# Kernel optimization log

Hardware: AMD Instinct MI355X
Metric: run time of the kernel (lower is better)

Reference implementation:

```python
import jax, jax.numpy as jnp
import numpy as np

B, A, N_IN, N_POINTS = 64, 256, 512, 2048


def _sq_cdist(u, v):
    # |u_i - v_j|^2 via expansion, abs() as in the torch original
    d = -2.0 * (u @ v.T) + (u * u).sum(1)[:, None] + (v * v).sum(1)[None, :]
    return jnp.abs(d)


def setup_inputs() -> dict:
    key = jax.random.key(0)
    k1, k2, k3, k4 = jax.random.split(key, 4)
    x = jax.random.normal(k1, (B, A, N_IN), dtype=jnp.float32)
    atom_mask = jax.random.bernoulli(k2, 0.8, (B, A))  # ragged valid-atom mask
    inducing_points = jax.random.normal(k3, (N_POINTS, N_IN), dtype=jnp.float32)
    gamma = (1.0 + 0.25 * jax.random.normal(k4, (N_IN,), dtype=jnp.float32)) * np.sqrt(N_IN).astype(np.float32)
    return {"x": x, "atom_mask": atom_mask, "inducing_points": inducing_points, "gamma": gamma}


def reference(x, atom_mask, inducing_points, gamma):
    b, a, n_in = x.shape
    m = atom_mask.astype(x.dtype)                      # [B, A]
    mf = m[..., None]                                  # [B, A, 1]
    n = m.sum()
    # masked mean / unbiased std over valid atoms (torch .std is ddof=1)
    mean = (x * mf).sum((0, 1)) / n                    # [n_in]
    var = (((x - mean) ** 2) * mf).sum((0, 1)) / (n - 1.0)
    std = jnp.sqrt(var) + 1e-5                         # [n_in]
    xn = (x - mean) / std * mf                         # zero out padded atoms

    g2 = gamma ** 2 + 0.001                            # [n_in]
    z = (xn / g2).reshape(b * a, n_in)                 # [N, n_in]
    zi = inducing_points / g2                          # [M, n_in]

    Kx = jnp.exp(-_sq_cdist(z, zi))                    # [N, M]
    Kind = jnp.exp(-_sq_cdist(zi, zi))                 # [M, M]
    Kinv = jnp.linalg.inv(Kind + 0.05 * jnp.eye(Kind.shape[0], dtype=x.dtype))

    t = Kx @ Kinv                                      # [N, M]
    x_new = ((t @ inducing_points) * std + mean).reshape(b, a, n_in) * mf
    var_out = (1.0 - (t * Kx).sum(-1)).reshape(b, a) * m
    return x_new, var_out
```

## Files before the change

kernel.cpp:

```cpp
#include <hip/hip_runtime.h>
#include <math.h>
#include <stdint.h>

namespace {

constexpr int NROW = 16384;
constexpr int NF   = 512;
constexpr int MIND = 2048;
constexpr float CC = 0.98f;

typedef _Float16 half8 __attribute__((ext_vector_type(8)));
typedef float floatx4 __attribute__((ext_vector_type(4)));

__device__ __forceinline__ void gload16(const void* g, void* l) {
  __builtin_amdgcn_global_load_lds(
      (__attribute__((address_space(1))) void*)g,
      (__attribute__((address_space(3))) void*)l, 16, 0, 0);
}

__global__ __launch_bounds__(256) void stats_kernel(
    const float* __restrict__ x, const int* __restrict__ mask,
    float* __restrict__ sum, float* __restrict__ sumsq, float* __restrict__ cnt)
{
  const int t = threadIdx.x;
  const int row0 = blockIdx.x * 64;
  float s0 = 0.f, s1 = 0.f, q0 = 0.f, q1 = 0.f, c = 0.f;
  for (int r = 0; r < 64; ++r) {
    const int row = row0 + r;
    const float m = (mask[row] != 0) ? 1.f : 0.f;
    const float v0 = x[(size_t)row * NF + t];
    const float v1 = x[(size_t)row * NF + t + 256];
    s0 += m * v0; q0 += m * v0 * v0;
    s1 += m * v1; q1 += m * v1 * v1;
    c += m;
  }
  atomicAdd(&sum[t], s0);        atomicAdd(&sum[t + 256], s1);
  atomicAdd(&sumsq[t], q0);      atomicAdd(&sumsq[t + 256], q1);
  if (t == 0) atomicAdd(cnt, c);
}

__global__ __launch_bounds__(256) void finalize_stats(
    const float* __restrict__ sum, const float* __restrict__ sumsq,
    const float* __restrict__ cnt, const float* __restrict__ gamma,
    float* __restrict__ meanv, float* __restrict__ stdv,
    float* __restrict__ zsv, float* __restrict__ giv)
{
  const int f = blockIdx.x * 256 + threadIdx.x;
  const float n = cnt[0];
  const float mu = sum[f] / n;
  const float var = (sumsq[f] - sum[f] * mu) / (n - 1.0f);
  const float sd = sqrtf(var) + 1e-5f;
  const float g = gamma[f];
  const float g2 = g * g + 0.001f;
  meanv[f] = mu;
  stdv[f]  = sd;
  zsv[f]   = 1.0f / (sd * g2);
  giv[f]   = 1.0f / g2;
}

__global__ __launch_bounds__(256) void make_z(
    const float* __restrict__ x, const int* __restrict__ mask,
    const float* __restrict__ ip, const float* __restrict__ meanv,
    const float* __restrict__ zsv, const float* __restrict__ giv,
    _Float16* __restrict__ Zh, _Float16* __restrict__ Zih,
    float* __restrict__ rnorm, float* __restrict__ cnorm)
{
  const int row = blockIdx.x;
  const int t = threadIdx.x;
  float v0, v1;
  if (row < NROW) {
    const float m = (mask[row] != 0) ? 1.f : 0.f;
    v0 = (x[(size_t)row * NF + t      ] - meanv[t      ]) * zsv[t      ] * m;
    v1 = (x[(size_t)row * NF + t + 256] - meanv[t + 256]) * zsv[t + 256] * m;
    const _Float16 h0 = (_Float16)v0, h1 = (_Float16)v1;
    Zh[(size_t)row * NF + t] = h0;
    Zh[(size_t)row * NF + t + 256] = h1;
    v0 = (float)h0; v1 = (float)h1;
  } else {
    const int r = row - NROW;
    v0 = ip[(size_t)r * NF + t      ] * giv[t      ];
    v1 = ip[(size_t)r * NF + t + 256] * giv[t + 256];
    const _Float16 h0 = (_Float16)v0, h1 = (_Float16)v1;
    Zih[(size_t)r * NF + t] = h0;
    Zih[(size_t)r * NF + t + 256] = h1;
    v0 = (float)h0; v1 = (float)h1;
  }
  float nrm = v0 * v0 + v1 * v1;
  #pragma unroll
  for (int off = 32; off; off >>= 1) nrm += __shfl_xor(nrm, off);
  __shared__ float red[4];
  if ((t & 63) == 0) red[t >> 6] = nrm;
  __syncthreads();
  if (t == 0) {
    const float s = red[0] + red[1] + red[2] + red[3];
    if (row < NROW) rnorm[row] = s; else cnorm[row - NROW] = s;
  }
}

template <int EPI>
__global__ __launch_bounds__(256) void mfma_gemm(
    const _Float16* __restrict__ A, const _Float16* __restrict__ B,
    int M, int N, int K,
    const float* __restrict__ rn, const float* __restrict__ cn,
    _Float16* __restrict__ DKout, float* __restrict__ Cf,
    const _Float16* __restrict__ DK, const float* __restrict__ u,
    float* __restrict__ varacc,
    const float* __restrict__ colsumR,
    const float* __restrict__ stdv, const float* __restrict__ meanv,
    const int* __restrict__ mask)
{
  __shared__ __align__(16) _Float16 As[128 * 32];
  __shared__ __align__(16) _Float16 Bs[128 * 32];
  const int tid = threadIdx.x;
  const int w = tid >> 6, L = tid & 63;
  const int wm = w >> 1, wn = w & 1;
  const int bn = blockIdx.x, bm = blockIdx.y;
  const int lq = L >> 4;
  const int lr = L & 15;

  floatx4 acc[4][4] = {};

  const _Float16* Ag = A + (size_t)(bm * 128) * K;
  const _Float16* Bg = B + (size_t)(bn * 128) * K;
  const int srow = w * 32 + (L >> 2);
  const int scol = (L & 3) * 8;

  for (int k0 = 0; k0 < K; k0 += 32) {
    #pragma unroll
    for (int t = 0; t < 2; ++t) {
      const int r = srow + t * 16;
      gload16(Ag + (size_t)r * K + k0 + scol, As + r * 32 + scol);
      gload16(Bg + (size_t)r * K + k0 + scol, Bs + r * 32 + scol);
    }
    __syncthreads();
    half8 af[4], bf[4];
    #pragma unroll
    for (int mi = 0; mi < 4; ++mi)
      af[mi] = *(const half8*)&As[(wm * 64 + mi * 16 + lr) * 32 + lq * 8];
    #pragma unroll
    for (int ni = 0; ni < 4; ++ni)
      bf[ni] = *(const half8*)&Bs[(wn * 64 + ni * 16 + lr) * 32 + lq * 8];
    #pragma unroll
    for (int mi = 0; mi < 4; ++mi)
      #pragma unroll
      for (int ni = 0; ni < 4; ++ni)
        acc[mi][ni] = __builtin_amdgcn_mfma_f32_16x16x32_f16(
            af[mi], bf[ni], acc[mi][ni], 0, 0, 0);
    __syncthreads();
  }

  const int grb = bm * 128 + wm * 64;
  const int gcb = bn * 128 + wn * 64;

  if constexpr (EPI == 2) {
    #pragma unroll
    for (int mi = 0; mi < 4; ++mi)
      #pragma unroll
      for (int e = 0; e < 4; ++e) {
        const int gr = grb + mi * 16 + lq * 4 + e;
        float partial = 0.f;
        #pragma unroll
        for (int ni = 0; ni < 4; ++ni) {
          const int gc = gcb + ni * 16 + lr;
          const float t = acc[mi][ni][e] + CC * u[gc];
          const float kx = CC + (float)DK[(size_t)gr * N + gc];
          partial += t * kx;
        }
        partial += __shfl_xor(partial, 1);
        partial += __shfl_xor(partial, 2);
        partial += __shfl_xor(partial, 4);
        partial += __shfl_xor(partial, 8);
        if (lr == 0) atomicAdd(&varacc[gr], partial);
      }
  } else if constexpr (EPI == 3) {
    #pragma unroll
    for (int mi = 0; mi < 4; ++mi)
      #pragma unroll
      for (int e = 0; e < 4; ++e) {
        const int gr = grb + mi * 16 + lq * 4 + e;
        const float mrow = (mask[gr] != 0) ? 1.f : 0.f;
        #pragma unroll
        for (int ni = 0; ni < 4; ++ni) {
          const int gc = gcb + ni * 16 + lr;
          const float v = acc[mi][ni][e] + CC * colsumR[gc];
          Cf[(size_t)gr * N + gc] = (v * stdv[gc] + meanv[gc]) * mrow;
        }
      }
  } else {
    #pragma unroll
    for (int mi = 0; mi < 4; ++mi)
      #pragma unroll
      for (int e = 0; e < 4; ++e) {
        const int gr = grb + mi * 16 + lq * 4 + e;
        const float rni = rn[gr];
        #pragma unroll
        for (int ni = 0; ni < 4; ++ni) {
          const int gc = gcb + ni * 16 + lr;
          const float d = rni + cn[gc] - 2.f * acc[mi][ni][e];
          float kx = expf(-fabsf(d));
          if constexpr (EPI == 0) {
            DKout[(size_t)gr * N + gc] = (_Float16)(kx - CC);
          } else {
            if (gr == gc) kx += 0.05f;
            Cf[(size_t)gr * N + gc] = kx;
          }
        }
      }
  }
}

__global__ __launch_bounds__(256) void gemm_f32(
    const float* __restrict__ A, const float* __restrict__ B,
    float* __restrict__ C, int M, int N, int K)
{
  constexpr int BM = 64, BN = 64, BK = 16;
  const int tid = threadIdx.x;
  const int tx = tid % 16, ty = tid / 16;
  const int bn = blockIdx.x, bm = blockIdx.y;
  __shared__ float As[BK][BM + 4];
  __shared__ float Bs[BK][BN + 4];
  float acc[4][4] = {};
  const float* Ag = A + (size_t)bm * BM * K;
  const float* Bg = B + bn * BN;
  for (int k0 = 0; k0 < K; k0 += BK) {
    {
      const int r = tid >> 2, c4 = (tid & 3) << 2;
      const float4 av = *(const float4*)(Ag + (size_t)r * K + k0 + c4);
      As[c4 + 0][r] = av.x; As[c4 + 1][r] = av.y;
      As[c4 + 2][r] = av.z; As[c4 + 3][r] = av.w;
      const int kr = tid / 16, nc = (tid % 16) << 2;
      *(float4*)&Bs[kr][nc] = *(const float4*)(Bg + (size_t)(k0 + kr) * N + nc);
    }
    __syncthreads();
    #pragma unroll
    for (int kk = 0; kk < BK; ++kk) {
      const float4 a4 = *(const float4*)&As[kk][ty * 4];
      const float4 b4 = *(const float4*)&Bs[kk][tx * 4];
      const float a[4] = {a4.x, a4.y, a4.z, a4.w};
      const float b[4] = {b4.x, b4.y, b4.z, b4.w};
      #pragma unroll
      for (int i = 0; i < 4; ++i)
        #pragma unroll
        for (int j = 0; j < 4; ++j) acc[i][j] += a[i] * b[j];
    }
    __syncthreads();
  }
  #pragma unroll
  for (int i = 0; i < 4; ++i) {
    float4 o4; o4.x = acc[i][0]; o4.y = acc[i][1]; o4.z = acc[i][2]; o4.w = acc[i][3];
    *(float4*)(C + (size_t)(bm * BM + ty * 4 + i) * N + bn * BN + tx * 4) = o4;
  }
}

__global__ __launch_bounds__(256) void gj_diag(
    float* __restrict__ A, float* __restrict__ P, int o)
{
  __shared__ float D[64][68];
  const int t = threadIdx.x;
  #pragma unroll
  for (int l = 0; l < 4; ++l) {
    const int v = t + l * 256;
    const int r = v >> 4, c4 = (v & 15) << 2;
    *(float4*)&D[r][c4] = *(const float4*)(A + (size_t)(o + r) * MIND + o + c4);
  }
  __syncthreads();
  const int i = t >> 2, c0 = (t & 3) * 16;
  for (int s = 0; s < 64; ++s) {
    const float p = 1.0f / D[s][s];
    if (t < 64 && t != s) D[s][t] *= p;
    __syncthreads();
    if (i != s) {
      const float f = D[i][s];
      #pragma unroll
      for (int c = c0; c < c0 + 16; c += 4) {
        float4 ds = *(const float4*)&D[s][c];
        float4 di = *(const float4*)&D[i][c];
        di.x -= f * ds.x; di.y -= f * ds.y; di.z -= f * ds.z; di.w -= f * ds.w;
        *(float4*)&D[i][c] = di;
      }
      if (s >= c0 && s < c0 + 16) D[i][s] = -f * p;
    }
    if (t == 0) D[s][s] = p;
    __syncthreads();
  }
  #pragma unroll
  for (int l = 0; l < 4; ++l) {
    const int v = t + l * 256;
    const int r = v >> 4, c4 = (v & 15) << 2;
    const float4 dv = *(const float4*)&D[r][c4];
    *(float4*)(P + r * 64 + c4) = dv;
    *(float4*)(A + (size_t)(o + r) * MIND + o + c4) = dv;
  }
}

__global__ __launch_bounds__(256) void gj_row(
    float* __restrict__ A, const float* __restrict__ P, int o)
{
  const int j0 = blockIdx.x * 64;
  if (j0 == o) return;
  __shared__ float Pt[64][68];
  __shared__ float Bt[64][68];
  const int t = threadIdx.x;
  #pragma unroll
  for (int l = 0; l < 4; ++l) {
    const int v = t + l * 256;
    const int r = v >> 4, c4 = (v & 15) << 2;
    const float4 pv = *(const float4*)(P + r * 64 + c4);
    Pt[c4 + 0][r] = pv.x; Pt[c4 + 1][r] = pv.y;
    Pt[c4 + 2][r] = pv.z; Pt[c4 + 3][r] = pv.w;
    *(float4*)&Bt[r][c4] = *(const float4*)(A + (size_t)(o + r) * MIND + j0 + c4);
  }
  __syncthreads();
  const int ty = t >> 4, tx = t & 15;
  float acc[4][4] = {};
  for (int s = 0; s < 64; ++s) {
    const float4 a4 = *(const float4*)&Pt[s][ty * 4];
    const float4 b4 = *(const float4*)&Bt[s][tx * 4];
    const float a[4] = {a4.x, a4.y, a4.z, a4.w};
    const float b[4] = {b4.x, b4.y, b4.z, b4.w};
    #pragma unroll
    for (int i = 0; i < 4; ++i)
      #pragma unroll
      for (int j = 0; j < 4; ++j) acc[i][j] += a[i] * b[j];
  }
  #pragma unroll
  for (int i = 0; i < 4; ++i) {
    float4 o4; o4.x = acc[i][0]; o4.y = acc[i][1]; o4.z = acc[i][2]; o4.w = acc[i][3];
    *(float4*)(A + (size_t)(o + ty * 4 + i) * MIND + j0 + tx * 4) = o4;
  }
}

__global__ __launch_bounds__(256) void gj_big(float* __restrict__ A, int o)
{
  const int j0 = blockIdx.x * 64, i0 = blockIdx.y * 64;
  if (i0 == o || j0 == o) return;
  __shared__ float Ct[64][68];
  __shared__ float Rw[64][68];
  const int t = threadIdx.x;
  #pragma unroll
  for (int l = 0; l < 4; ++l) {
    const int v = t + l * 256;
    const int r = v >> 4, c4 = (v & 15) << 2;
    const float4 av = *(const float4*)(A + (size_t)(i0 + r) * MIND + o + c4);
    Ct[c4 + 0][r] = av.x; Ct[c4 + 1][r] = av.y;
    Ct[c4 + 2][r] = av.z; Ct[c4 + 3][r] = av.w;
    *(float4*)&Rw[r][c4] = *(const float4*)(A + (size_t)(o + r) * MIND + j0 + c4);
  }
  __syncthreads();
  const int ty = t >> 4, tx = t & 15;
  float acc[4][4] = {};
  for (int k = 0; k < 64; ++k) {
    const float4 a4 = *(const float4*)&Ct[k][ty * 4];
    const float4 b4 = *(const float4*)&Rw[k][tx * 4];
    const float a[4] = {a4.x, a4.y, a4.z, a4.w};
    const float b[4] = {b4.x, b4.y, b4.z, b4.w};
    #pragma unroll
    for (int i = 0; i < 4; ++i)
      #pragma unroll
      for (int j = 0; j < 4; ++j) acc[i][j] += a[i] * b[j];
  }
  #pragma unroll
  for (int i = 0; i < 4; ++i) {
    float* cp = A + (size_t)(i0 + ty * 4 + i) * MIND + j0 + tx * 4;
    float4 cv = *(const float4*)cp;
    cv.x -= acc[i][0]; cv.y -= acc[i][1]; cv.z -= acc[i][2]; cv.w -= acc[i][3];
    *(float4*)cp = cv;
  }
}

__global__ __launch_bounds__(256) void gj_col(
    float* __restrict__ A, const float* __restrict__ P, int o)
{
  const int i0 = blockIdx.x * 64;
  if (i0 == o) return;
  __shared__ float Ot[64][68];
  __shared__ float Pl[64][68];
  const int t = threadIdx.x;
  #pragma unroll
  for (int l = 0; l < 4; ++l) {
    const int v = t + l * 256;
    const int r = v >> 4, c4 = (v & 15) << 2;
    const float4 av = *(const float4*)(A + (size_t)(i0 + r) * MIND + o + c4);
    Ot[c4 + 0][r] = av.x; Ot[c4 + 1][r] = av.y;
    Ot[c4 + 2][r] = av.z; Ot[c4 + 3][r] = av.w;
    *(float4*)&Pl[r][c4] = *(const float4*)(P + r * 64 + c4);
  }
  __syncthreads();
  const int ty = t >> 4, tx = t & 15;
  float acc[4][4] = {};
  for (int s = 0; s < 64; ++s) {
    const float4 a4 = *(const float4*)&Ot[s][ty * 4];
    const float4 b4 = *(const float4*)&Pl[s][tx * 4];
    const float a[4] = {a4.x, a4.y, a4.z, a4.w};
    const float b[4] = {b4.x, b4.y, b4.z, b4.w};
    #pragma unroll
    for (int i = 0; i < 4; ++i)
      #pragma unroll
      for (int j = 0; j < 4; ++j) acc[i][j] += a[i] * b[j];
  }
  #pragma unroll
  for (int i = 0; i < 4; ++i) {
    float4 o4;
    o4.x = -acc[i][0]; o4.y = -acc[i][1]; o4.z = -acc[i][2]; o4.w = -acc[i][3];
    *(float4*)(A + (size_t)(i0 + ty * 4 + i) * MIND + o + tx * 4) = o4;
  }
}

__global__ __launch_bounds__(256) void rowsum_kernel(
    const float* __restrict__ Ai, float* __restrict__ u)
{
  const int row = blockIdx.x * 4 + (threadIdx.x >> 6);
  const int lane = threadIdx.x & 63;
  float s = 0.f;
  for (int c = lane; c < MIND; c += 64) s += Ai[(size_t)row * MIND + c];
  #pragma unroll
  for (int off = 32; off; off >>= 1) s += __shfl_xor(s, off);
  if (lane == 0) u[row] = s;
}

typedef _Float16 half4v __attribute__((ext_vector_type(4)));
__global__ __launch_bounds__(256) void cast_half4(
    const float* __restrict__ s, _Float16* __restrict__ d)
{
  const int i = (blockIdx.x * 256 + threadIdx.x) * 4;
  const float4 v = *(const float4*)(s + i);
  half4v h; h.x = (_Float16)v.x; h.y = (_Float16)v.y;
  h.z = (_Float16)v.z; h.w = (_Float16)v.w;
  *(half4v*)(d + i) = h;
}

__global__ __launch_bounds__(256) void transpose_cast(
    const float* __restrict__ R, _Float16* __restrict__ Rt)
{
  __shared__ float T[64][65];
  const int j0 = blockIdx.x * 64;
  const int f0 = blockIdx.y * 64;
  const int t = threadIdx.x;
  #pragma unroll
  for (int l = 0; l < 16; ++l) {
    const int idx = t + l * 256;
    T[idx >> 6][idx & 63] = R[(size_t)(j0 + (idx >> 6)) * NF + f0 + (idx & 63)];
  }
  __syncthreads();
  #pragma unroll
  for (int l = 0; l < 16; ++l) {
    const int idx = t + l * 256;
    const int fr = idx >> 6, jc = idx & 63;
    Rt[(size_t)(f0 + fr) * MIND + j0 + jc] = (_Float16)T[jc][fr];
  }
}

__global__ __launch_bounds__(256) void colsum_kernel(
    const float* __restrict__ R, float* __restrict__ cs)
{
  const int b = blockIdx.x;
  const int t = threadIdx.x;
  float s0 = 0.f, s1 = 0.f;
  for (int r = 0; r < 64; ++r) {
    s0 += R[(size_t)(b * 64 + r) * NF + t];
    s1 += R[(size_t)(b * 64 + r) * NF + t + 256];
  }
  atomicAdd(&cs[t], s0); atomicAdd(&cs[t + 256], s1);
}

__global__ __launch_bounds__(256) void var_finalize(
    const float* __restrict__ varacc, const int* __restrict__ mask,
    float* __restrict__ outv)
{
  const int i = blockIdx.x * 256 + threadIdx.x;
  const float m = (mask[i] != 0) ? 1.f : 0.f;
  outv[i] = (1.0f - varacc[i]) * m;
}

}

extern "C" void kernel_launch(void* const* d_in, const int* in_sizes, int n_in,
                              void* d_out, int out_size, void* d_ws, size_t ws_size,
                              hipStream_t stream)
{
  (void)in_sizes; (void)n_in; (void)out_size; (void)ws_size;
  const float* x     = (const float*)d_in[0];
  const int*   mask  = (const int*)d_in[1];
  const float* ip    = (const float*)d_in[2];
  const float* gamma = (const float*)d_in[3];
  float* out = (float*)d_out;

  float* w       = (float*)d_ws;
  float* sum     = w;
  float* sumsq   = w + 512;
  float* cnt     = w + 1024;
  float* varacc  = w + 1536;
  float* colsumR = w + 17920;
  float* meanv   = w + 18432;
  float* stdv    = w + 18944;
  float* zsv     = w + 19456;
  float* giv     = w + 19968;
  float* rnorm   = w + 20480;
  float* cnorm   = w + 36864;
  float* u       = w + 38912;
  float* Ai      = w + 40960;
  float* Pd      = w + 40960 + 4194304 - 4096;
  float* R       = w + 4235264;
  float* Pdiag   = w + 5283840;
  _Float16* hb   = (_Float16*)(w + 5283840 + 4096);
  _Float16* Zh   = hb;
  _Float16* Zih  = hb + 8388608;
  _Float16* DK   = hb + 9437184;
  _Float16* Kih  = hb + 42991616;
  _Float16* Rt   = hb + 47185920;
  (void)Pd;

  hipMemsetAsync(w, 0, 18432 * sizeof(float), stream);

  stats_kernel<<<256, 256, 0, stream>>>(x, mask, sum, sumsq, cnt);
  finalize_stats<<<2, 256, 0, stream>>>(sum, sumsq, cnt, gamma, meanv, stdv, zsv, giv);
  make_z<<<NROW + MIND, 256, 0, stream>>>(x, mask, ip, meanv, zsv, giv, Zh, Zih, rnorm, cnorm);

  mfma_gemm<0><<<dim3(MIND / 128, NROW / 128), 256, 0, stream>>>(
      Zh, Zih, NROW, MIND, NF, rnorm, cnorm,
      DK, nullptr, nullptr, nullptr, nullptr, nullptr, nullptr, nullptr, nullptr);
  mfma_gemm<1><<<dim3(MIND / 128, MIND / 128), 256, 0, stream>>>(
      Zih, Zih, MIND, MIND, NF, cnorm, cnorm,
      nullptr, Ai, nullptr, nullptr, nullptr, nullptr, nullptr, nullptr, nullptr);

  for (int o = 0; o < MIND; o += 64) {
    gj_diag<<<1, 256, 0, stream>>>(Ai, Pdiag, o);
    gj_row<<<32, 256, 0, stream>>>(Ai, Pdiag, o);
    gj_big<<<dim3(32, 32), 256, 0, stream>>>(Ai, o);
    gj_col<<<32, 256, 0, stream>>>(Ai, Pdiag, o);
  }

  gemm_f32<<<dim3(NF / 64, MIND / 64), 256, 0, stream>>>(Ai, ip, R, MIND, NF, MIND);
  transpose_cast<<<dim3(MIND / 64, NF / 64), 256, 0, stream>>>(R, Rt);
  colsum_kernel<<<MIND / 64, 256, 0, stream>>>(R, colsumR);
  rowsum_kernel<<<MIND / 4, 256, 0, stream>>>(Ai, u);
  cast_half4<<<(MIND * MIND) / 1024, 256, 0, stream>>>(Ai, Kih);

  mfma_gemm<2><<<dim3(MIND / 128, NROW / 128), 256, 0, stream>>>(
      DK, Kih, NROW, MIND, MIND, nullptr, nullptr,
      nullptr, nullptr, DK, u, varacc, nullptr, nullptr, nullptr, nullptr);

  mfma_gemm<3><<<dim3(NF / 128, NROW / 128), 256, 0, stream>>>(
      DK, Rt, NROW, NF, MIND, nullptr, nullptr,
      nullptr, out, nullptr, nullptr, nullptr, colsumR, stdv, meanv, mask);

  var_finalize<<<NROW / 256, 256, 0, stream>>>(varacc, mask, out + (size_t)NROW * NF);
}
```

Measured before the change: 2.440 ms.

## Fuse Gauss-Jordan row/col/update steps and compute next diagonal inverse inside update

Restructures the blocked Gauss-Jordan inversion from four launches per pivot step into a prep kernel and a fused apply kernel. The prep kernel computes the column-times-pivot product and saves the pivot row strip. The apply kernel writes the pivot row, the column and the trailing updates in one launch. The block that owns the next diagonal tile also inverts it in place, so the separate single-block diagonal launch disappears. This cuts launch count and serial gaps, at the cost of one block doing the serial 64-step elimination inside the large grid, which may lengthen that grid's tail.

```diff
diff --git a/kernel.cpp b/kernel.cpp
--- a/kernel.cpp
+++ b/kernel.cpp
@@ -252,9 +252,11 @@
   }
 }
 
+
 __global__ __launch_bounds__(256) void gj_diag(
-    float* __restrict__ A, float* __restrict__ P, int o)
-{
+    float* __restrict__ A, float* __restrict__ Pall, int k)
+{
+  const int o = k * 64;
   __shared__ float D[64][68];
   const int t = threadIdx.x;
   #pragma unroll
@@ -283,6 +285,7 @@
     if (t == 0) D[s][s] = p;
     __syncthreads();
   }
+  float* P = Pall + k * 4096;
   #pragma unroll
   for (int l = 0; l < 4; ++l) {
     const int v = t + l * 256;
@@ -293,29 +296,43 @@
   }
 }
 
-__global__ __launch_bounds__(256) void gj_row(
-    float* __restrict__ A, const float* __restrict__ P, int o)
-{
-  const int j0 = blockIdx.x * 64;
-  if (j0 == o) return;
-  __shared__ float Pt[64][68];
-  __shared__ float Bt[64][68];
+__global__ __launch_bounds__(256) void gj_prep(
+    const float* __restrict__ A, const float* __restrict__ Pall,
+    float* __restrict__ CP, float* __restrict__ Bsave, int k)
+{
+  const int o = k * 64;
   const int t = threadIdx.x;
+  if (blockIdx.x >= 32) {
+    const int j0 = (blockIdx.x - 32) * 64;
+    #pragma unroll
+    for (int l = 0; l < 4; ++l) {
+      const int v = t + l * 256;
+      const int r = v >> 4, c4 = (v & 15) << 2;
+      *(float4*)(Bsave + r * MIND + j0 + c4) =
+          *(const float4*)(A + (size_t)(o + r) * MIND + j0 + c4);
+    }
+    return;
+  }
+  const int i0 = blockIdx.x * 64;
+  if (i0 == o) return;
+  const float* P = Pall + k * 4096;
+  __shared__ float At[64][68];
+  __shared__ float Pl[64][68];
   #pragma unroll
   for (int l = 0; l < 4; ++l) {
     const int v = t + l * 256;
     const int r = v >> 4, c4 = (v & 15) << 2;
-    const float4 pv = *(const float4*)(P + r * 64 + c4);
-    Pt[c4 + 0][r] = pv.x; Pt[c4 + 1][r] = pv.y;
-    Pt[c4 + 2][r] = pv.z; Pt[c4 + 3][r] = pv.w;
-    *(float4*)&Bt[r][c4] = *(const float4*)(A + (size_t)(o + r) * MIND + j0 + c4);
+    const float4 av = *(const float4*)(A + (size_t)(i0 + r) * MIND + o + c4);
+    At[c4 + 0][r] = av.x; At[c4 + 1][r] = av.y;
+    At[c4 + 2][r] = av.z; At[c4 + 3][r] = av.w;
+    *(float4*)&Pl[r][c4] = *(const float4*)(P + r * 64 + c4);
   }
   __syncthreads();
   const int ty = t >> 4, tx = t & 15;
   float acc[4][4] = {};
   for (int s = 0; s < 64; ++s) {
-    const float4 a4 = *(const float4*)&Pt[s][ty * 4];
-    const float4 b4 = *(const float4*)&Bt[s][tx * 4];
+    const float4 a4 = *(const float4*)&At[s][ty * 4];
+    const float4 b4 = *(const float4*)&Pl[s][tx * 4];
     const float a[4] = {a4.x, a4.y, a4.z, a4.w};
     const float b[4] = {b4.x, b4.y, b4.z, b4.w};
     #pragma unroll
@@ -326,71 +343,53 @@
   #pragma unroll
   for (int i = 0; i < 4; ++i) {
     float4 o4; o4.x = acc[i][0]; o4.y = acc[i][1]; o4.z = acc[i][2]; o4.w = acc[i][3];
-    *(float4*)(A + (size_t)(o + ty * 4 + i) * MIND + j0 + tx * 4) = o4;
-  }
-}
-
-__global__ __launch_bounds__(256) void gj_big(float* __restrict__ A, int o)
-{
-  const int j0 = blockIdx.x * 64, i0 = blockIdx.y * 64;
-  if (i0 == o || j0 == o) return;
-  __shared__ float Ct[64][68];
-  __shared__ float Rw[64][68];
+    *(float4*)(CP + (i0 + ty * 4 + i) * 64 + tx * 4) = o4;
+  }
+}
+
+__global__ __launch_bounds__(256) void gj_apply(
+    float* __restrict__ A, float* __restrict__ Pall,
+    const float* __restrict__ CP, const float* __restrict__ Bsave, int k)
+{
+  const int o = k * 64;
+  const int i0 = blockIdx.y * 64, j0 = blockIdx.x * 64;
   const int t = threadIdx.x;
+
+  if (i0 == o && j0 == o) return;
+
+  if (j0 == o) {
+    #pragma unroll
+    for (int l = 0; l < 4; ++l) {
+      const int v = t + l * 256;
+      const int r = v >> 4, c4 = (v & 15) << 2;
+      float4 x = *(const float4*)(CP + (i0 + r) * 64 + c4);
+      x.x = -x.x; x.y = -x.y; x.z = -x.z; x.w = -x.w;
+      *(float4*)(A + (size_t)(i0 + r) * MIND + o + c4) = x;
+    }
+    return;
+  }
+
+  __shared__ float S1[64 * 68];
+  __shared__ float S2[64 * 68];
+  #define DD(r, c) S1[(r) * 68 + (c)]
+
+  const bool isrow = (i0 == o);
+  const float* Lsrc = isrow ? (Pall + k * 4096) : (CP + i0 * 64);
   #pragma unroll
   for (int l = 0; l < 4; ++l) {
     const int v = t + l * 256;
     const int r = v >> 4, c4 = (v & 15) << 2;
-    const float4 av = *(const float4*)(A + (size_t)(i0 + r) * MIND + o + c4);
-    Ct[c4 + 0][r] = av.x; Ct[c4 + 1][r] = av.y;
-    Ct[c4 + 2][r] = av.z; Ct[c4 + 3][r] = av.w;
-    *(float4*)&Rw[r][c4] = *(const float4*)(A + (size_t)(o + r) * MIND + j0 + c4);
-  }
-  __syncthreads();
-  const int ty = t >> 4, tx = t & 15;
-  float acc[4][4] = {};
-  for (int k = 0; k < 64; ++k) {
-    const float4 a4 = *(const float4*)&Ct[k][ty * 4];
-    const float4 b4 = *(const float4*)&Rw[k][tx * 4];
-    const float a[4] = {a4.x, a4.y, a4.z, a4.w};
-    const float b[4] = {b4.x, b4.y, b4.z, b4.w};
-    #pragma unroll
-    for (int i = 0; i < 4; ++i)
-      #pragma unroll
-      for (int j = 0; j < 4; ++j) acc[i][j] += a[i] * b[j];
-  }
-  #pragma unroll
-  for (int i = 0; i < 4; ++i) {
-    float* cp = A + (size_t)(i0 + ty * 4 + i) * MIND + j0 + tx * 4;
-    float4 cv = *(const float4*)cp;
-    cv.x -= acc[i][0]; cv.y -= acc[i][1]; cv.z -= acc[i][2]; cv.w -= acc[i][3];
-    *(float4*)cp = cv;
-  }
-}
-
-__global__ __launch_bounds__(256) void gj_col(
-    float* __restrict__ A, const float* __restrict__ P, int o)
-{
-  const int i0 = blockIdx.x * 64;
-  if (i0 == o) return;
-  __shared__ float Ot[64][68];
-  __shared__ float Pl[64][68];
-  const int t = threadIdx.x;
-  #pragma unroll
-  for (int l = 0; l < 4; ++l) {
-    const int v = t + l * 256;
-    const int r = v >> 4, c4 = (v & 15) << 2;
-    const float4 av = *(const float4*)(A + (size_t)(i0 + r) * MIND + o + c4);
-    Ot[c4 + 0][r] = av.x; Ot[c4 + 1][r] = av.y;
-    Ot[c4 + 2][r] = av.z; Ot[c4 + 3][r] = av.w;
-    *(float4*)&Pl[r][c4] = *(const float4*)(P + r * 64 + c4);
+    const float4 lv = *(const float4*)(Lsrc + r * 64 + c4);
+    S1[(c4 + 0) * 68 + r] = lv.x; S1[(c4 + 1) * 68 + r] = lv.y;
+    S1[(c4 + 2) * 68 + r] = lv.z; S1[(c4 + 3) * 68 + r] = lv.w;
+    *(float4*)&S2[r * 68 + c4] = *(const float4*)(Bsave + r * MIND + j0 + c4);
   }
   __syncthreads();
   const int ty = t >> 4, tx = t & 15;
   float acc[4][4] = {};
   for (int s = 0; s < 64; ++s) {
-    const float4 a4 = *(const float4*)&Ot[s][ty * 4];
-    const float4 b4 = *(const float4*)&Pl[s][tx * 4];
+    const float4 a4 = *(const float4*)&S1[s * 68 + ty * 4];
+    const float4 b4 = *(const float4*)&S2[s * 68 + tx * 4];
     const float a[4] = {a4.x, a4.y, a4.z, a4.w};
     const float b[4] = {b4.x, b4.y, b4.z, b4.w};
     #pragma unroll
@@ -398,12 +397,67 @@
       #pragma unroll
       for (int j = 0; j < 4; ++j) acc[i][j] += a[i] * b[j];
   }
+
+  if (isrow) {
+    #pragma unroll
+    for (int i = 0; i < 4; ++i) {
+      float4 o4; o4.x = acc[i][0]; o4.y = acc[i][1]; o4.z = acc[i][2]; o4.w = acc[i][3];
+      *(float4*)(A + (size_t)(o + ty * 4 + i) * MIND + j0 + tx * 4) = o4;
+    }
+    return;
+  }
+
+  const bool isdiagnext = (i0 == o + 64) && (j0 == o + 64);
+  if (!isdiagnext) {
+    #pragma unroll
+    for (int i = 0; i < 4; ++i) {
+      float* cp = A + (size_t)(i0 + ty * 4 + i) * MIND + j0 + tx * 4;
+      float4 cv = *(const float4*)cp;
+      cv.x -= acc[i][0]; cv.y -= acc[i][1]; cv.z -= acc[i][2]; cv.w -= acc[i][3];
+      *(float4*)cp = cv;
+    }
+    return;
+  }
+
+  __syncthreads();
   #pragma unroll
   for (int i = 0; i < 4; ++i) {
-    float4 o4;
-    o4.x = -acc[i][0]; o4.y = -acc[i][1]; o4.z = -acc[i][2]; o4.w = -acc[i][3];
-    *(float4*)(A + (size_t)(i0 + ty * 4 + i) * MIND + o + tx * 4) = o4;
-  }
+    const float4 cv = *(const float4*)(A + (size_t)(i0 + ty * 4 + i) * MIND + j0 + tx * 4);
+    DD(ty * 4 + i, tx * 4 + 0) = cv.x - acc[i][0];
+    DD(ty * 4 + i, tx * 4 + 1) = cv.y - acc[i][1];
+    DD(ty * 4 + i, tx * 4 + 2) = cv.z - acc[i][2];
+    DD(ty * 4 + i, tx * 4 + 3) = cv.w - acc[i][3];
+  }
+  __syncthreads();
+  const int di = t >> 2, c0 = (t & 3) * 16;
+  for (int s = 0; s < 64; ++s) {
+    const float p = 1.0f / DD(s, s);
+    if (t < 64 && t != s) DD(s, t) *= p;
+    __syncthreads();
+    if (di != s) {
+      const float f = DD(di, s);
+      #pragma unroll
+      for (int c = c0; c < c0 + 16; c += 4) {
+        float4 ds = *(const float4*)&DD(s, c);
+        float4 dv = *(const float4*)&DD(di, c);
+        dv.x -= f * ds.x; dv.y -= f * ds.y; dv.z -= f * ds.z; dv.w -= f * ds.w;
+        *(float4*)&DD(di, c) = dv;
+      }
+      if (s >= c0 && s < c0 + 16) DD(di, s) = -f * p;
+    }
+    if (t == 0) DD(s, s) = p;
+    __syncthreads();
+  }
+  float* Pn = Pall + (k + 1) * 4096;
+  #pragma unroll
+  for (int l = 0; l < 4; ++l) {
+    const int v = t + l * 256;
+    const int r = v >> 4, c4 = (v & 15) << 2;
+    const float4 dv = *(const float4*)&DD(r, c4);
+    *(float4*)(Pn + r * 64 + c4) = dv;
+    *(float4*)(A + (size_t)(i0 + r) * MIND + j0 + c4) = dv;
+  }
+  #undef DD
 }
 
 __global__ __launch_bounds__(256) void rowsum_kernel(
@@ -499,16 +553,16 @@
   float* cnorm   = w + 36864;
   float* u       = w + 38912;
   float* Ai      = w + 40960;
-  float* Pd      = w + 40960 + 4194304 - 4096;
   float* R       = w + 4235264;
-  float* Pdiag   = w + 5283840;
-  _Float16* hb   = (_Float16*)(w + 5283840 + 4096);
+  float* Pall    = w + 5283840;
+  float* CP      = w + 5414912;
+  float* Bsave   = w + 5545984;
+  _Float16* hb   = (_Float16*)(w + 5677056);
   _Float16* Zh   = hb;
   _Float16* Zih  = hb + 8388608;
   _Float16* DK   = hb + 9437184;
   _Float16* Kih  = hb + 42991616;
   _Float16* Rt   = hb + 47185920;
-  (void)Pd;
 
   hipMemsetAsync(w, 0, 18432 * sizeof(float), stream);
 
@@ -523,11 +577,11 @@
       Zih, Zih, MIND, MIND, NF, cnorm, cnorm,
       nullptr, Ai, nullptr, nullptr, nullptr, nullptr, nullptr, nullptr, nullptr);
 
-  for (int o = 0; o < MIND; o += 64) {
-    gj_diag<<<1, 256, 0, stream>>>(Ai, Pdiag, o);
-    gj_row<<<32, 256, 0, stream>>>(Ai, Pdiag, o);
-    gj_big<<<dim3(32, 32), 256, 0, stream>>>(Ai, o);
-    gj_col<<<32, 256, 0, stream>>>(Ai, Pdiag, o);
+  gj_diag<<<1, 256, 0, stream>>>(Ai, Pall, 0);
+  gj_prep<<<64, 256, 0, stream>>>(Ai, Pall, CP, Bsave, 0);
+  for (int k = 0; k < 32; ++k) {
+    gj_apply<<<dim3(32, 32), 256, 0, stream>>>(Ai, Pall, CP, Bsave, k);
+    if (k < 31) gj_prep<<<64, 256, 0, stream>>>(Ai, Pall, CP, Bsave, k + 1);
   }
 
   gemm_f32<<<dim3(NF / 64, MIND / 64), 256, 0, stream>>>(Ai, ip, R, MIND, NF, MIND);
```

Result: faster. 2.170 ms (-11.1%).
